# Performance work log

Hardware: AMD Instinct MI355X
Metric: run time of the kernel (lower is better)

The kernel has to match this reference:

```python
import jax, jax.numpy as jnp
import numpy as np

B, D = 32, 2048


def setup_inputs() -> dict:
    key = jax.random.key(0)
    ks = jax.random.split(key, 7)
    # torch init: weights ~ N(0, 0.1^2); biases default Linear uniform(-1/sqrt(D), 1/sqrt(D))
    bound = 1.0 / np.sqrt(D)
    return {
        "x": jax.random.normal(ks[0], (B, D), dtype=jnp.float32),
        "Wq": 0.1 * jax.random.normal(ks[1], (D, D), dtype=jnp.float32),
        "bq": jax.random.uniform(ks[2], (D,), minval=-bound, maxval=bound, dtype=jnp.float32),
        "Wk": 0.1 * jax.random.normal(ks[3], (D, D), dtype=jnp.float32),
        "bk": jax.random.uniform(ks[4], (D,), minval=-bound, maxval=bound, dtype=jnp.float32),
        "Wv": 0.1 * jax.random.normal(ks[5], (D, D), dtype=jnp.float32),
        "bv": jax.random.uniform(ks[6], (D,), minval=-bound, maxval=bound, dtype=jnp.float32),
    }


def reference(x, Wq, bq, Wk, bk, Wv, bv):
    # q,k,v: [B, D] feature-wise projections (torch Linear: x @ W^T + b)
    q = x @ Wq.T + bq
    k = x @ Wk.T + bk
    v = x @ Wv.T + bv
    # rank-1 outer product scores[b,i,j] = q[b,i] * k[b,j]  -> [B, D, D]
    scores = q[:, :, None] * k[:, None, :]
    # softmax over dim=1 (as in the original F.softmax(..., dim=1))
    weights = jax.nn.softmax(scores, axis=1)
    # weighted V sum: out[b,i] = sum_j weights[b,i,j] * v[b,j]  -> [B, D]
    out = jnp.einsum("bij,bj->bi", weights, v)
    return out
```

## Files before the change

kernel.cpp:

```cpp
#include <hip/hip_runtime.h>
#include <math.h>


#define D 2048
#define BATCH 32
#define SEGF 68
#define NPART 4

#define PART_STRIDE 196608
#define KDP_OFF 786432
#define NP_OFF  925696

#define L2E 1.4426950408889634f

typedef short s16x8 __attribute__((ext_vector_type(8)));
typedef float f32x4 __attribute__((ext_vector_type(4)));

union FragU { s16x8 v; unsigned u[4]; };

__device__ __forceinline__ float fast_exp2(float x) {
#if __has_builtin(__builtin_amdgcn_exp2f)
  return __builtin_amdgcn_exp2f(x);
#else
  return exp2f(x);
#endif
}
__device__ __forceinline__ unsigned pack_rne(float a, float b) {
  unsigned ua = __float_as_uint(a), ub = __float_as_uint(b);
  ua = ua + 0x7FFFu + ((ua >> 16) & 1u);
  ub = ub + 0x7FFFu + ((ub >> 16) & 1u);
  return (ua >> 16) | (ub & 0xFFFF0000u);
}
__device__ __forceinline__ void pack8(const float4& fa, const float4& fb,
                                      FragU& h) {
  h.u[0] = pack_rne(fa.x, fa.y);
  h.u[1] = pack_rne(fa.z, fa.w);
  h.u[2] = pack_rne(fb.x, fb.y);
  h.u[3] = pack_rne(fb.z, fb.w);
}
__device__ __forceinline__ float sum_parts(const float* __restrict__ ws,
                                           size_t o) {
  float s0 = ws[o] + ws[o + PART_STRIDE];
  float s1 = ws[o + 2 * PART_STRIDE] + ws[o + 3 * PART_STRIDE];
  return s0 + s1;
}

__global__ __launch_bounds__(256, 2) void k1_proj(
    const float* __restrict__ x, const float* __restrict__ Wq,
    const float* __restrict__ Wk, const float* __restrict__ Wv,
    float* __restrict__ ws) {
  __shared__ float red[4][512];
  const int tid = threadIdx.x;
  const int lane = tid & 63, wv = tid >> 6;
  const int tile = blockIdx.x >> 2, kq = blockIdx.x & 3;
  const int m = tile >> 7, lr = (tile & 127) * 16;
  const float* W = (m == 0) ? Wq : (m == 1) ? Wk : Wv;

  const int kbase = kq * 512 + wv * 128 + (lane >> 4) * 8;
  const float* ap = W + (size_t)(lr + (lane & 15)) * D + kbase;
  const float* xp0 = x + (size_t)(lane & 15) * D + kbase;
  const float* xp1 = xp0 + 16 * D;

  float4 fa[4], fb[4], x0a[4], x0b[4], x1a[4], x1b[4];
#pragma unroll
  for (int s = 0; s < 4; ++s) {
    const int off = s * 32;
    fa[s] = *(const float4*)(ap + off);
    fb[s] = *(const float4*)(ap + off + 4);
    x0a[s] = *(const float4*)(xp0 + off);
    x0b[s] = *(const float4*)(xp0 + off + 4);
    x1a[s] = *(const float4*)(xp1 + off);
    x1b[s] = *(const float4*)(xp1 + off + 4);
  }

  f32x4 acc0 = {0.f, 0.f, 0.f, 0.f}, acc1 = {0.f, 0.f, 0.f, 0.f};
#pragma unroll
  for (int s = 0; s < 4; ++s) {
    FragU Ah, Bh0, Bh1;
    pack8(fa[s], fb[s], Ah);
    pack8(x0a[s], x0b[s], Bh0);
    pack8(x1a[s], x1b[s], Bh1);
    acc0 = __builtin_amdgcn_mfma_f32_16x16x32_bf16(Ah.v, Bh0.v, acc0, 0, 0, 0);
    acc1 = __builtin_amdgcn_mfma_f32_16x16x32_bf16(Ah.v, Bh1.v, acc1, 0, 0, 0);
  }
  const int col = lane & 15, rq = (lane >> 4) * 4;
#pragma unroll
  for (int r = 0; r < 4; ++r) {
    red[wv][col * 16 + rq + r] = acc0[r];
    red[wv][(col + 16) * 16 + rq + r] = acc1[r];
  }
  __syncthreads();
  float* part = ws + (size_t)kq * PART_STRIDE + (size_t)m * 65536;
#pragma unroll
  for (int i = tid; i < 512; i += 256) {
    float s = (red[0][i] + red[1][i]) + (red[2][i] + red[3][i]);
    part[(size_t)(i >> 4) * D + lr + (i & 15)] = s;
  }
}

__global__ __launch_bounds__(512, 8) void k3_dz(float* __restrict__ ws,
                                                const float* __restrict__ bq,
                                                const float* __restrict__ bk,
                                                const float* __restrict__ bv) {
  __shared__ float qs[2048];
  __shared__ float zs[512];
  __shared__ float rmx[8], rmn[8];
  __shared__ int cnt[2];
  const int bx = blockIdx.x, t = threadIdx.x;
  const int b = bx >> 5, jc = bx & 31;
  if (t == 0) { cnt[0] = 0; cnt[1] = 0; }

  const size_t qb = (size_t)b * D;
  float4 p0 = ((const float4*)(ws + qb))[t];
  float4 p1 = ((const float4*)(ws + PART_STRIDE + qb))[t];
  float4 p2 = ((const float4*)(ws + 2 * PART_STRIDE + qb))[t];
  float4 p3 = ((const float4*)(ws + 3 * PART_STRIDE + qb))[t];
  float4 bb = ((const float4*)bq)[t];
  float4 qv = {(p0.x + p1.x) + (p2.x + p3.x) + bb.x,
               (p0.y + p1.y) + (p2.y + p3.y) + bb.y,
               (p0.z + p1.z) + (p2.z + p3.z) + bb.z,
               (p0.w + p1.w) + (p2.w + p3.w) + bb.w};
  *(float4*)&qs[t * 4] = qv;
  float mx = fmaxf(fmaxf(qv.x, qv.y), fmaxf(qv.z, qv.w));
  float mn = fminf(fminf(qv.x, qv.y), fminf(qv.z, qv.w));
#pragma unroll
  for (int off = 32; off; off >>= 1) {
    mx = fmaxf(mx, __shfl_down(mx, off));
    mn = fminf(mn, __shfl_down(mn, off));
  }
  if ((t & 63) == 0) { rmx[t >> 6] = mx; rmn[t >> 6] = mn; }
  __syncthreads();
  mx = rmx[0]; mn = rmn[0];
#pragma unroll
  for (int w = 1; w < 8; ++w) {
    mx = fmaxf(mx, rmx[w]);
    mn = fminf(mn, rmn[w]);
  }

  const int jl = t & 63, ih = t >> 6;
  const int j = jc * 64 + jl;
  const float k2 = (sum_parts(ws, 65536 + qb + j) + bk[j]) * L2E;
  const float m2 = (k2 >= 0.f) ? k2 * mx : k2 * mn;
  const float nm2 = -m2;
  const float* qp = qs + ih * 256;
  float z0 = 0.f, z1 = 0.f, z2 = 0.f, z3 = 0.f;
#pragma unroll 8
  for (int i = 0; i < 256; i += 4) {
    float4 q4 = *(const float4*)&qp[i];
    z0 += fast_exp2(fmaf(q4.x, k2, nm2));
    z1 += fast_exp2(fmaf(q4.y, k2, nm2));
    z2 += fast_exp2(fmaf(q4.z, k2, nm2));
    z3 += fast_exp2(fmaf(q4.w, k2, nm2));
  }
  zs[t] = (z0 + z1) + (z2 + z3);
  __syncthreads();

  float2* kdp = (float2*)(ws + KDP_OFF) + ((size_t)b * 32 + jc) * SEGF;
  if (t < 64) {
    float Z = ((zs[t] + zs[t + 64]) + (zs[t + 128] + zs[t + 192])) +
              ((zs[t + 256] + zs[t + 320]) + (zs[t + 384] + zs[t + 448]));
    float v = sum_parts(ws, 131072 + qb + j) + bv[j];
    float d = __log2f(fabsf(v) / Z) - m2;
    int slot;
    if (v >= 0.f) slot = atomicAdd(&cnt[0], 1);
    else          slot = (SEGF - 1) - atomicAdd(&cnt[1], 1);
    kdp[slot] = make_float2(k2, d);
  }
  __syncthreads();
  const int npos = cnt[0];
  if (t < 4) kdp[npos + t] = make_float2(0.f, -1e30f);
  if (t == 0) ((int*)(ws + NP_OFF))[b * 32 + jc] = npos;
}

__global__ __launch_bounds__(512, 8) void k4_out(const float* __restrict__ ws,
                                                 const float* __restrict__ bq,
                                                 float* __restrict__ out) {
  __shared__ float2 kd[32 * SEGF];
  __shared__ int np[32];
  __shared__ float rs[512];
  const int bx = blockIdx.x, t = threadIdx.x;
  const int b = bx >> 5, ic = bx & 31;

  const float4* src = (const float4*)((const float2*)(ws + KDP_OFF) +
                                      (size_t)b * 32 * SEGF);
  for (int idx = t; idx < (32 * SEGF) / 2; idx += 512)
    ((float4*)kd)[idx] = src[idx];
  if (t < 32) np[t] = ((const int*)(ws + NP_OFF))[b * 32 + t];

  const int il = t & 63, jh = t >> 6;
  const int i = ic * 64 + il;
  const size_t io = (size_t)b * D + i;
  const float qi = sum_parts(ws, io) + bq[i];
  __syncthreads();

  float p0 = 0.f, p1 = 0.f, p2 = 0.f, p3 = 0.f;
  float n0 = 0.f, n1 = 0.f, n2 = 0.f, n3 = 0.f;
#pragma unroll
  for (int s = jh * 4; s < jh * 4 + 4; ++s) {
    const float2* seg = kd + s * SEGF;
    const int npos = np[s];
    const int pe = (npos + 3) & ~3;
    const int ns = (npos + 4) & ~3;
    for (int jj = 0; jj < pe; jj += 4) {
      float4 t0 = *(const float4*)&seg[jj];
      float4 t1 = *(const float4*)&seg[jj + 2];
      p0 += fast_exp2(fmaf(qi, t0.x, t0.y));
      p1 += fast_exp2(fmaf(qi, t0.z, t0.w));
      p2 += fast_exp2(fmaf(qi, t1.x, t1.y));
      p3 += fast_exp2(fmaf(qi, t1.z, t1.w));
    }
    for (int jj = ns; jj < SEGF; jj += 4) {
      float4 t0 = *(const float4*)&seg[jj];
      float4 t1 = *(const float4*)&seg[jj + 2];
      n0 += fast_exp2(fmaf(qi, t0.x, t0.y));
      n1 += fast_exp2(fmaf(qi, t0.z, t0.w));
      n2 += fast_exp2(fmaf(qi, t1.x, t1.y));
      n3 += fast_exp2(fmaf(qi, t1.z, t1.w));
    }
  }
  rs[t] = ((p0 + p1) + (p2 + p3)) - ((n0 + n1) + (n2 + n3));
  __syncthreads();
  if (t < 64)
    out[io] = ((rs[il] + rs[il + 64]) + (rs[il + 128] + rs[il + 192])) +
              ((rs[il + 256] + rs[il + 320]) + (rs[il + 384] + rs[il + 448]));
}

extern "C" void kernel_launch(void* const* d_in, const int* in_sizes, int n_in,
                              void* d_out, int out_size, void* d_ws, size_t ws_size,
                              hipStream_t stream) {
  (void)in_sizes; (void)n_in; (void)out_size; (void)ws_size;
  const float* x  = (const float*)d_in[0];
  const float* Wq = (const float*)d_in[1];
  const float* bq = (const float*)d_in[2];
  const float* Wk = (const float*)d_in[3];
  const float* bk = (const float*)d_in[4];
  const float* Wv = (const float*)d_in[5];
  const float* bv = (const float*)d_in[6];
  float* ws  = (float*)d_ws;
  float* out = (float*)d_out;

  k1_proj<<<1536, 256, 0, stream>>>(x, Wq, Wk, Wv, ws);
  k3_dz<<<1024, 512, 0, stream>>>(ws, bq, bk, bv);
  k4_out<<<1024, 512, 0, stream>>>(ws, bq, out);
}
```

Measured before the change: 141.6 us.

## Finalize projections once and compact sign-split key lists per batch globally

A new k2_fin kernel sums the four split-K partials and adds the biases once, writing final q, scaled k and v. It also writes per-chunk q max/min so later kernels no longer re-reduce partials. k3 now appends (k,d) pairs into per-batch positive and negative global arrays using global atomic counters, replacing padded per-segment slots of 68 entries. k4 streams these compact lists straight from global memory with a uniform loop split across waves, removing the LDS staging and the padding waste. The cost is an extra kernel launch, contended global atomics, and cache reads in place of LDS in the hot exp loop.

```diff
diff --git a/kernel.cpp b/kernel.cpp
--- a/kernel.cpp
+++ b/kernel.cpp
@@ -4,12 +4,16 @@
 
 #define D 2048
 #define BATCH 32
-#define SEGF 68
 #define NPART 4
 
 #define PART_STRIDE 196608
-#define KDP_OFF 786432
-#define NP_OFF  925696
+#define QF_OFF  786432
+#define KF_OFF  851968
+#define VF_OFF  917504
+#define QMM_OFF 983040
+#define CNT_OFF 983552
+#define PKD_OFF 983616
+#define NKD_OFF 1114688
 
 #define L2E 1.4426950408889634f
 
@@ -37,12 +41,6 @@
   h.u[1] = pack_rne(fa.z, fa.w);
   h.u[2] = pack_rne(fb.x, fb.y);
   h.u[3] = pack_rne(fb.z, fb.w);
-}
-__device__ __forceinline__ float sum_parts(const float* __restrict__ ws,
-                                           size_t o) {
-  float s0 = ws[o] + ws[o + PART_STRIDE];
-  float s1 = ws[o + 2 * PART_STRIDE] + ws[o + 3 * PART_STRIDE];
-  return s0 + s1;
 }
 
 __global__ __launch_bounds__(256, 2) void k1_proj(
@@ -98,55 +96,68 @@
   }
 }
 
-__global__ __launch_bounds__(512, 8) void k3_dz(float* __restrict__ ws,
-                                                const float* __restrict__ bq,
-                                                const float* __restrict__ bk,
-                                                const float* __restrict__ bv) {
-  __shared__ float qs[2048];
+__global__ __launch_bounds__(256) void k2_fin(float* __restrict__ ws,
+                                              const float* __restrict__ bq,
+                                              const float* __restrict__ bk,
+                                              const float* __restrict__ bv) {
+  __shared__ float smx[4], smn[4];
+  const int id = blockIdx.x, t = threadIdx.x;
+  const int m = id >> 8, r = id & 255, b = r >> 3, c = r & 7;
+  const int i = c * 256 + t;
+  const size_t e = (size_t)m * 65536 + (size_t)b * D + i;
+  float s = (ws[e] + ws[e + PART_STRIDE]) +
+            (ws[e + 2 * PART_STRIDE] + ws[e + 3 * PART_STRIDE]);
+  if (m == 0) {
+    s += bq[i];
+    ws[QF_OFF + (size_t)b * D + i] = s;
+    float mx = s, mn = s;
+#pragma unroll
+    for (int off = 32; off; off >>= 1) {
+      mx = fmaxf(mx, __shfl_down(mx, off));
+      mn = fminf(mn, __shfl_down(mn, off));
+    }
+    if ((t & 63) == 0) { smx[t >> 6] = mx; smn[t >> 6] = mn; }
+    __syncthreads();
+    if (t == 0) {
+      mx = fmaxf(fmaxf(smx[0], smx[1]), fmaxf(smx[2], smx[3]));
+      mn = fminf(fminf(smn[0], smn[1]), fminf(smn[2], smn[3]));
+      float* qm = ws + QMM_OFF + (size_t)(b * 8 + c) * 2;
+      qm[0] = mx; qm[1] = mn;
+    }
+    if (c == 0 && t < 2) ((int*)(ws + CNT_OFF))[b * 2 + t] = 0;
+  } else if (m == 1) {
+    ws[KF_OFF + (size_t)b * D + i] = (s + bk[i]) * L2E;
+  } else {
+    ws[VF_OFF + (size_t)b * D + i] = s + bv[i];
+  }
+}
+
+__global__ __launch_bounds__(512, 8) void k3_z(
+    const float* __restrict__ qf, const float* __restrict__ kf,
+    const float* __restrict__ vf, const float* __restrict__ qmm,
+    int* __restrict__ cnt, float2* __restrict__ pkd,
+    float2* __restrict__ nkd) {
   __shared__ float zs[512];
-  __shared__ float rmx[8], rmn[8];
-  __shared__ int cnt[2];
   const int bx = blockIdx.x, t = threadIdx.x;
   const int b = bx >> 5, jc = bx & 31;
-  if (t == 0) { cnt[0] = 0; cnt[1] = 0; }
-
-  const size_t qb = (size_t)b * D;
-  float4 p0 = ((const float4*)(ws + qb))[t];
-  float4 p1 = ((const float4*)(ws + PART_STRIDE + qb))[t];
-  float4 p2 = ((const float4*)(ws + 2 * PART_STRIDE + qb))[t];
-  float4 p3 = ((const float4*)(ws + 3 * PART_STRIDE + qb))[t];
-  float4 bb = ((const float4*)bq)[t];
-  float4 qv = {(p0.x + p1.x) + (p2.x + p3.x) + bb.x,
-               (p0.y + p1.y) + (p2.y + p3.y) + bb.y,
-               (p0.z + p1.z) + (p2.z + p3.z) + bb.z,
-               (p0.w + p1.w) + (p2.w + p3.w) + bb.w};
-  *(float4*)&qs[t * 4] = qv;
-  float mx = fmaxf(fmaxf(qv.x, qv.y), fmaxf(qv.z, qv.w));
-  float mn = fminf(fminf(qv.x, qv.y), fminf(qv.z, qv.w));
-#pragma unroll
-  for (int off = 32; off; off >>= 1) {
-    mx = fmaxf(mx, __shfl_down(mx, off));
-    mn = fminf(mn, __shfl_down(mn, off));
-  }
-  if ((t & 63) == 0) { rmx[t >> 6] = mx; rmn[t >> 6] = mn; }
-  __syncthreads();
-  mx = rmx[0]; mn = rmn[0];
+  const int jl = t & 63;
+  const int ih = __builtin_amdgcn_readfirstlane(t >> 6);
+  const int j = jc * 64 + jl;
+  const float k2 = kf[(size_t)b * D + j];
+  const float* qm = qmm + b * 16;
+  float mx = qm[0], mn = qm[1];
 #pragma unroll
   for (int w = 1; w < 8; ++w) {
-    mx = fmaxf(mx, rmx[w]);
-    mn = fminf(mn, rmn[w]);
-  }
-
-  const int jl = t & 63, ih = t >> 6;
-  const int j = jc * 64 + jl;
-  const float k2 = (sum_parts(ws, 65536 + qb + j) + bk[j]) * L2E;
+    mx = fmaxf(mx, qm[2 * w]);
+    mn = fminf(mn, qm[2 * w + 1]);
+  }
   const float m2 = (k2 >= 0.f) ? k2 * mx : k2 * mn;
   const float nm2 = -m2;
-  const float* qp = qs + ih * 256;
+  const float* qp = qf + (size_t)b * D + ih * 256;
   float z0 = 0.f, z1 = 0.f, z2 = 0.f, z3 = 0.f;
 #pragma unroll 8
-  for (int i = 0; i < 256; i += 4) {
-    float4 q4 = *(const float4*)&qp[i];
+  for (int i2 = 0; i2 < 256; i2 += 4) {
+    float4 q4 = *(const float4*)(qp + i2);
     z0 += fast_exp2(fmaf(q4.x, k2, nm2));
     z1 += fast_exp2(fmaf(q4.y, k2, nm2));
     z2 += fast_exp2(fmaf(q4.z, k2, nm2));
@@ -154,75 +165,74 @@
   }
   zs[t] = (z0 + z1) + (z2 + z3);
   __syncthreads();
-
-  float2* kdp = (float2*)(ws + KDP_OFF) + ((size_t)b * 32 + jc) * SEGF;
   if (t < 64) {
     float Z = ((zs[t] + zs[t + 64]) + (zs[t + 128] + zs[t + 192])) +
               ((zs[t + 256] + zs[t + 320]) + (zs[t + 384] + zs[t + 448]));
-    float v = sum_parts(ws, 131072 + qb + j) + bv[j];
-    float d = __log2f(fabsf(v) / Z) - m2;
-    int slot;
-    if (v >= 0.f) slot = atomicAdd(&cnt[0], 1);
-    else          slot = (SEGF - 1) - atomicAdd(&cnt[1], 1);
-    kdp[slot] = make_float2(k2, d);
-  }
-  __syncthreads();
-  const int npos = cnt[0];
-  if (t < 4) kdp[npos + t] = make_float2(0.f, -1e30f);
-  if (t == 0) ((int*)(ws + NP_OFF))[b * 32 + jc] = npos;
-}
-
-__global__ __launch_bounds__(512, 8) void k4_out(const float* __restrict__ ws,
-                                                 const float* __restrict__ bq,
-                                                 float* __restrict__ out) {
-  __shared__ float2 kd[32 * SEGF];
-  __shared__ int np[32];
+    const float v = vf[(size_t)b * D + j];
+    const float d = __log2f(fabsf(v) / Z) - m2;
+    if (v >= 0.f) {
+      int s = atomicAdd(&cnt[b * 2], 1);
+      pkd[(size_t)b * D + s] = make_float2(k2, d);
+    } else {
+      int s = atomicAdd(&cnt[b * 2 + 1], 1);
+      nkd[(size_t)b * D + s] = make_float2(k2, d);
+    }
+  }
+}
+
+__global__ __launch_bounds__(512, 8) void k4_out(
+    const float* __restrict__ qf, const int* __restrict__ cnt,
+    const float2* __restrict__ pkd, const float2* __restrict__ nkd,
+    float* __restrict__ out) {
   __shared__ float rs[512];
   const int bx = blockIdx.x, t = threadIdx.x;
   const int b = bx >> 5, ic = bx & 31;
-
-  const float4* src = (const float4*)((const float2*)(ws + KDP_OFF) +
-                                      (size_t)b * 32 * SEGF);
-  for (int idx = t; idx < (32 * SEGF) / 2; idx += 512)
-    ((float4*)kd)[idx] = src[idx];
-  if (t < 32) np[t] = ((const int*)(ws + NP_OFF))[b * 32 + t];
-
-  const int il = t & 63, jh = t >> 6;
+  const int il = t & 63;
+  const int jh = __builtin_amdgcn_readfirstlane(t >> 6);
   const int i = ic * 64 + il;
-  const size_t io = (size_t)b * D + i;
-  const float qi = sum_parts(ws, io) + bq[i];
-  __syncthreads();
+  const float qi = qf[(size_t)b * D + i];
+  const int npos = cnt[b * 2], nneg = cnt[b * 2 + 1];
+  const float2* pp = pkd + (size_t)b * D;
+  const float2* np = nkd + (size_t)b * D;
 
   float p0 = 0.f, p1 = 0.f, p2 = 0.f, p3 = 0.f;
+  const int GP = npos >> 2;
+  for (int g = jh; g < GP; g += 8) {
+    const float4* e4 = (const float4*)(pp + g * 4);
+    float4 a = e4[0], c4 = e4[1];
+    p0 += fast_exp2(fmaf(qi, a.x, a.y));
+    p1 += fast_exp2(fmaf(qi, a.z, a.w));
+    p2 += fast_exp2(fmaf(qi, c4.x, c4.y));
+    p3 += fast_exp2(fmaf(qi, c4.z, c4.w));
+  }
+  if (jh == 0) {
+    for (int jj = GP * 4; jj < npos; ++jj) {
+      float2 e = pp[jj];
+      p0 += fast_exp2(fmaf(qi, e.x, e.y));
+    }
+  }
   float n0 = 0.f, n1 = 0.f, n2 = 0.f, n3 = 0.f;
-#pragma unroll
-  for (int s = jh * 4; s < jh * 4 + 4; ++s) {
-    const float2* seg = kd + s * SEGF;
-    const int npos = np[s];
-    const int pe = (npos + 3) & ~3;
-    const int ns = (npos + 4) & ~3;
-    for (int jj = 0; jj < pe; jj += 4) {
-      float4 t0 = *(const float4*)&seg[jj];
-      float4 t1 = *(const float4*)&seg[jj + 2];
-      p0 += fast_exp2(fmaf(qi, t0.x, t0.y));
-      p1 += fast_exp2(fmaf(qi, t0.z, t0.w));
-      p2 += fast_exp2(fmaf(qi, t1.x, t1.y));
-      p3 += fast_exp2(fmaf(qi, t1.z, t1.w));
-    }
-    for (int jj = ns; jj < SEGF; jj += 4) {
-      float4 t0 = *(const float4*)&seg[jj];
-      float4 t1 = *(const float4*)&seg[jj + 2];
-      n0 += fast_exp2(fmaf(qi, t0.x, t0.y));
-      n1 += fast_exp2(fmaf(qi, t0.z, t0.w));
-      n2 += fast_exp2(fmaf(qi, t1.x, t1.y));
-      n3 += fast_exp2(fmaf(qi, t1.z, t1.w));
+  const int GN = nneg >> 2;
+  for (int g = jh; g < GN; g += 8) {
+    const float4* e4 = (const float4*)(np + g * 4);
+    float4 a = e4[0], c4 = e4[1];
+    n0 += fast_exp2(fmaf(qi, a.x, a.y));
+    n1 += fast_exp2(fmaf(qi, a.z, a.w));
+    n2 += fast_exp2(fmaf(qi, c4.x, c4.y));
+    n3 += fast_exp2(fmaf(qi, c4.z, c4.w));
+  }
+  if (jh == 1) {
+    for (int jj = GN * 4; jj < nneg; ++jj) {
+      float2 e = np[jj];
+      n0 += fast_exp2(fmaf(qi, e.x, e.y));
     }
   }
   rs[t] = ((p0 + p1) + (p2 + p3)) - ((n0 + n1) + (n2 + n3));
   __syncthreads();
   if (t < 64)
-    out[io] = ((rs[il] + rs[il + 64]) + (rs[il + 128] + rs[il + 192])) +
-              ((rs[il + 256] + rs[il + 320]) + (rs[il + 384] + rs[il + 448]));
+    out[(size_t)b * D + ic * 64 + t] =
+        ((rs[t] + rs[t + 64]) + (rs[t + 128] + rs[t + 192])) +
+        ((rs[t + 256] + rs[t + 320]) + (rs[t + 384] + rs[t + 448]));
 }
 
 extern "C" void kernel_launch(void* const* d_in, const int* in_sizes, int n_in,
@@ -240,6 +250,12 @@
   float* out = (float*)d_out;
 
   k1_proj<<<1536, 256, 0, stream>>>(x, Wq, Wk, Wv, ws);
-  k3_dz<<<1024, 512, 0, stream>>>(ws, bq, bk, bv);
-  k4_out<<<1024, 512, 0, stream>>>(ws, bq, out);
-}
+  k2_fin<<<768, 256, 0, stream>>>(ws, bq, bk, bv);
+  k3_z<<<1024, 512, 0, stream>>>(ws + QF_OFF, ws + KF_OFF, ws + VF_OFF,
+                                 ws + QMM_OFF, (int*)(ws + CNT_OFF),
+                                 (float2*)(ws + PKD_OFF),
+                                 (float2*)(ws + NKD_OFF));
+  k4_out<<<1024, 512, 0, stream>>>(ws + QF_OFF, (const int*)(ws + CNT_OFF),
+                                   (const float2*)(ws + PKD_OFF),
+                                   (const float2*)(ws + NKD_OFF), out);
+}
```

Result: slower. 544.6 us (+284.6%).

## Register-block two columns per thread and compact sign-partitioned k/d segments

Applied to the files above, without the earlier changes.

The Z kernel now has each thread handle two j columns, so each shared q load feeds two exp pipelines. Positive/negative partitioning uses a wavefront ballot with mbcnt instead of LDS atomics, writing 64-entry segments with no padding sentinels. The output kernel processes two i rows per thread over half as many blocks, reusing each LDS k/d load for both rows and handling the single mixed group with per-element predication. This cuts LDS traffic per exp and removes atomics, at the cost of more registers and lower declared occupancy in k4.

```diff
diff --git a/kernel.cpp b/kernel.cpp
--- a/kernel.cpp
+++ b/kernel.cpp
@@ -4,12 +4,11 @@
 
 #define D 2048
 #define BATCH 32
-#define SEGF 68
 #define NPART 4
 
 #define PART_STRIDE 196608
-#define KDP_OFF 786432
-#define NP_OFF  925696
+#define PKD_OFF 786432
+#define NPT_OFF 917504
 
 #define L2E 1.4426950408889634f
 
@@ -24,6 +23,10 @@
 #else
   return exp2f(x);
 #endif
+}
+__device__ __forceinline__ int bits_below(unsigned long long m) {
+  return __builtin_amdgcn_mbcnt_hi((unsigned)(m >> 32),
+         __builtin_amdgcn_mbcnt_lo((unsigned)m, 0));
 }
 __device__ __forceinline__ unsigned pack_rne(float a, float b) {
   unsigned ua = __float_as_uint(a), ub = __float_as_uint(b);
@@ -98,19 +101,18 @@
   }
 }
 
-__global__ __launch_bounds__(512, 8) void k3_dz(float* __restrict__ ws,
-                                                const float* __restrict__ bq,
-                                                const float* __restrict__ bk,
-                                                const float* __restrict__ bv) {
+__global__ __launch_bounds__(512, 8) void k3_z(float* __restrict__ ws,
+                                               const float* __restrict__ bq,
+                                               const float* __restrict__ bk,
+                                               const float* __restrict__ bv) {
   __shared__ float qs[2048];
-  __shared__ float zs[512];
+  __shared__ float zs[1024];
+  __shared__ float ks2[64], ms2[64];
   __shared__ float rmx[8], rmn[8];
-  __shared__ int cnt[2];
   const int bx = blockIdx.x, t = threadIdx.x;
   const int b = bx >> 5, jc = bx & 31;
-  if (t == 0) { cnt[0] = 0; cnt[1] = 0; }
-
   const size_t qb = (size_t)b * D;
+
   float4 p0 = ((const float4*)(ws + qb))[t];
   float4 p1 = ((const float4*)(ws + PART_STRIDE + qb))[t];
   float4 p2 = ((const float4*)(ws + 2 * PART_STRIDE + qb))[t];
@@ -137,92 +139,138 @@
     mn = fminf(mn, rmn[w]);
   }
 
-  const int jl = t & 63, ih = t >> 6;
-  const int j = jc * 64 + jl;
-  const float k2 = (sum_parts(ws, 65536 + qb + j) + bk[j]) * L2E;
-  const float m2 = (k2 >= 0.f) ? k2 * mx : k2 * mn;
-  const float nm2 = -m2;
-  const float* qp = qs + ih * 256;
-  float z0 = 0.f, z1 = 0.f, z2 = 0.f, z3 = 0.f;
+  const int jp = t & 31, ih = t >> 5;
+  const int j0 = jc * 64 + jp, j1 = j0 + 32;
+  const float k2a = (sum_parts(ws, 65536 + qb + j0) + bk[j0]) * L2E;
+  const float k2b = (sum_parts(ws, 65536 + qb + j1) + bk[j1]) * L2E;
+  const float m2a = (k2a >= 0.f) ? k2a * mx : k2a * mn;
+  const float m2b = (k2b >= 0.f) ? k2b * mx : k2b * mn;
+  if (ih == 0) {
+    ks2[jp] = k2a; ks2[32 + jp] = k2b;
+    ms2[jp] = m2a; ms2[32 + jp] = m2b;
+  }
+  const float na = -m2a, nb = -m2b;
+  const float* qp = qs + ih * 128;
+  float za0 = 0.f, za1 = 0.f, za2 = 0.f, za3 = 0.f;
+  float zb0 = 0.f, zb1 = 0.f, zb2 = 0.f, zb3 = 0.f;
 #pragma unroll 8
-  for (int i = 0; i < 256; i += 4) {
-    float4 q4 = *(const float4*)&qp[i];
-    z0 += fast_exp2(fmaf(q4.x, k2, nm2));
-    z1 += fast_exp2(fmaf(q4.y, k2, nm2));
-    z2 += fast_exp2(fmaf(q4.z, k2, nm2));
-    z3 += fast_exp2(fmaf(q4.w, k2, nm2));
-  }
-  zs[t] = (z0 + z1) + (z2 + z3);
-  __syncthreads();
-
-  float2* kdp = (float2*)(ws + KDP_OFF) + ((size_t)b * 32 + jc) * SEGF;
+  for (int i2 = 0; i2 < 128; i2 += 4) {
+    float4 q4 = *(const float4*)&qp[i2];
+    za0 += fast_exp2(fmaf(q4.x, k2a, na));
+    za1 += fast_exp2(fmaf(q4.y, k2a, na));
+    za2 += fast_exp2(fmaf(q4.z, k2a, na));
+    za3 += fast_exp2(fmaf(q4.w, k2a, na));
+    zb0 += fast_exp2(fmaf(q4.x, k2b, nb));
+    zb1 += fast_exp2(fmaf(q4.y, k2b, nb));
+    zb2 += fast_exp2(fmaf(q4.z, k2b, nb));
+    zb3 += fast_exp2(fmaf(q4.w, k2b, nb));
+  }
+  zs[ih * 64 + jp]      = (za0 + za1) + (za2 + za3);
+  zs[ih * 64 + 32 + jp] = (zb0 + zb1) + (zb2 + zb3);
+  __syncthreads();
+
   if (t < 64) {
-    float Z = ((zs[t] + zs[t + 64]) + (zs[t + 128] + zs[t + 192])) +
-              ((zs[t + 256] + zs[t + 320]) + (zs[t + 384] + zs[t + 448]));
-    float v = sum_parts(ws, 131072 + qb + j) + bv[j];
-    float d = __log2f(fabsf(v) / Z) - m2;
-    int slot;
-    if (v >= 0.f) slot = atomicAdd(&cnt[0], 1);
-    else          slot = (SEGF - 1) - atomicAdd(&cnt[1], 1);
-    kdp[slot] = make_float2(k2, d);
-  }
-  __syncthreads();
-  const int npos = cnt[0];
-  if (t < 4) kdp[npos + t] = make_float2(0.f, -1e30f);
-  if (t == 0) ((int*)(ws + NP_OFF))[b * 32 + jc] = npos;
-}
-
-__global__ __launch_bounds__(512, 8) void k4_out(const float* __restrict__ ws,
+    float Z = 0.f;
+#pragma unroll
+    for (int h = 0; h < 16; ++h) Z += zs[h * 64 + t];
+    const int j = jc * 64 + t;
+    const float v = sum_parts(ws, 131072 + qb + j) + bv[j];
+    const float d = __log2f(fabsf(v) / Z) - ms2[t];
+    const unsigned long long msk = __ballot(v >= 0.f);
+    const int npos = __popcll(msk);
+    const int slot = (v >= 0.f) ? bits_below(msk) : 63 - bits_below(~msk);
+    float2* dst = (float2*)(ws + PKD_OFF) + ((size_t)b * 32 + jc) * 64;
+    dst[slot] = make_float2(ks2[t], d);
+    if (t == 0) ((int*)(ws + NPT_OFF))[b * 32 + jc] = npos;
+  }
+}
+
+__global__ __launch_bounds__(512, 4) void k4_out(const float* __restrict__ ws,
                                                  const float* __restrict__ bq,
                                                  float* __restrict__ out) {
-  __shared__ float2 kd[32 * SEGF];
+  __shared__ float2 kd[2048];
   __shared__ int np[32];
-  __shared__ float rs[512];
+  __shared__ float rs[128 * 9];
   const int bx = blockIdx.x, t = threadIdx.x;
-  const int b = bx >> 5, ic = bx & 31;
-
-  const float4* src = (const float4*)((const float2*)(ws + KDP_OFF) +
-                                      (size_t)b * 32 * SEGF);
-  for (int idx = t; idx < (32 * SEGF) / 2; idx += 512)
-    ((float4*)kd)[idx] = src[idx];
-  if (t < 32) np[t] = ((const int*)(ws + NP_OFF))[b * 32 + t];
+  const int b = bx >> 4, ic = bx & 15;
+  const size_t qb = (size_t)b * D;
+
+  const float4* src = (const float4*)((const float2*)(ws + PKD_OFF) +
+                                      (size_t)b * 2048);
+  ((float4*)kd)[t] = src[t];
+  ((float4*)kd)[t + 512] = src[t + 512];
+  if (t < 32) np[t] = ((const int*)(ws + NPT_OFF))[b * 32 + t];
 
   const int il = t & 63, jh = t >> 6;
-  const int i = ic * 64 + il;
-  const size_t io = (size_t)b * D + i;
-  const float qi = sum_parts(ws, io) + bq[i];
-  __syncthreads();
-
-  float p0 = 0.f, p1 = 0.f, p2 = 0.f, p3 = 0.f;
-  float n0 = 0.f, n1 = 0.f, n2 = 0.f, n3 = 0.f;
-#pragma unroll
-  for (int s = jh * 4; s < jh * 4 + 4; ++s) {
-    const float2* seg = kd + s * SEGF;
-    const int npos = np[s];
-    const int pe = (npos + 3) & ~3;
-    const int ns = (npos + 4) & ~3;
-    for (int jj = 0; jj < pe; jj += 4) {
-      float4 t0 = *(const float4*)&seg[jj];
-      float4 t1 = *(const float4*)&seg[jj + 2];
-      p0 += fast_exp2(fmaf(qi, t0.x, t0.y));
-      p1 += fast_exp2(fmaf(qi, t0.z, t0.w));
-      p2 += fast_exp2(fmaf(qi, t1.x, t1.y));
-      p3 += fast_exp2(fmaf(qi, t1.z, t1.w));
+  const int i0 = ic * 128 + il, i1 = i0 + 64;
+  const float qi0 = sum_parts(ws, qb + i0) + bq[i0];
+  const float qi1 = sum_parts(ws, qb + i1) + bq[i1];
+  __syncthreads();
+
+  float pa0 = 0.f, pa1 = 0.f, pa2 = 0.f, pa3 = 0.f;
+  float pb0 = 0.f, pb1 = 0.f, pb2 = 0.f, pb3 = 0.f;
+  float na0 = 0.f, na1 = 0.f, na2 = 0.f, na3 = 0.f;
+  float nb0 = 0.f, nb1 = 0.f, nb2 = 0.f, nb3 = 0.f;
+#pragma unroll
+  for (int s4 = 0; s4 < 4; ++s4) {
+    const int s = jh * 4 + s4;
+    const float4* seg = (const float4*)(kd + s * 64);
+    const int npos = np[s], gb = npos >> 2;
+    for (int g = 0; g < gb; ++g) {
+      float4 a = seg[g * 2], c = seg[g * 2 + 1];
+      pa0 += fast_exp2(fmaf(qi0, a.x, a.y));
+      pa1 += fast_exp2(fmaf(qi0, a.z, a.w));
+      pa2 += fast_exp2(fmaf(qi0, c.x, c.y));
+      pa3 += fast_exp2(fmaf(qi0, c.z, c.w));
+      pb0 += fast_exp2(fmaf(qi1, a.x, a.y));
+      pb1 += fast_exp2(fmaf(qi1, a.z, a.w));
+      pb2 += fast_exp2(fmaf(qi1, c.x, c.y));
+      pb3 += fast_exp2(fmaf(qi1, c.z, c.w));
     }
-    for (int jj = ns; jj < SEGF; jj += 4) {
-      float4 t0 = *(const float4*)&seg[jj];
-      float4 t1 = *(const float4*)&seg[jj + 2];
-      n0 += fast_exp2(fmaf(qi, t0.x, t0.y));
-      n1 += fast_exp2(fmaf(qi, t0.z, t0.w));
-      n2 += fast_exp2(fmaf(qi, t1.x, t1.y));
-      n3 += fast_exp2(fmaf(qi, t1.z, t1.w));
+    if (gb < 16) {
+      {
+        float4 a = seg[gb * 2], c = seg[gb * 2 + 1];
+        const int base = gb * 4;
+        float ea0 = fast_exp2(fmaf(qi0, a.x, a.y));
+        float ea1 = fast_exp2(fmaf(qi0, a.z, a.w));
+        float ea2 = fast_exp2(fmaf(qi0, c.x, c.y));
+        float ea3 = fast_exp2(fmaf(qi0, c.z, c.w));
+        float eb0 = fast_exp2(fmaf(qi1, a.x, a.y));
+        float eb1 = fast_exp2(fmaf(qi1, a.z, a.w));
+        float eb2 = fast_exp2(fmaf(qi1, c.x, c.y));
+        float eb3 = fast_exp2(fmaf(qi1, c.z, c.w));
+        if (base + 0 < npos) { pa0 += ea0; pb0 += eb0; }
+        else                 { na0 += ea0; nb0 += eb0; }
+        if (base + 1 < npos) { pa1 += ea1; pb1 += eb1; }
+        else                 { na1 += ea1; nb1 += eb1; }
+        if (base + 2 < npos) { pa2 += ea2; pb2 += eb2; }
+        else                 { na2 += ea2; nb2 += eb2; }
+        if (base + 3 < npos) { pa3 += ea3; pb3 += eb3; }
+        else                 { na3 += ea3; nb3 += eb3; }
+      }
+      for (int g = gb + 1; g < 16; ++g) {
+        float4 a = seg[g * 2], c = seg[g * 2 + 1];
+        na0 += fast_exp2(fmaf(qi0, a.x, a.y));
+        na1 += fast_exp2(fmaf(qi0, a.z, a.w));
+        na2 += fast_exp2(fmaf(qi0, c.x, c.y));
+        na3 += fast_exp2(fmaf(qi0, c.z, c.w));
+        nb0 += fast_exp2(fmaf(qi1, a.x, a.y));
+        nb1 += fast_exp2(fmaf(qi1, a.z, a.w));
+        nb2 += fast_exp2(fmaf(qi1, c.x, c.y));
+        nb3 += fast_exp2(fmaf(qi1, c.z, c.w));
+      }
     }
   }
-  rs[t] = ((p0 + p1) + (p2 + p3)) - ((n0 + n1) + (n2 + n3));
-  __syncthreads();
-  if (t < 64)
-    out[io] = ((rs[il] + rs[il + 64]) + (rs[il + 128] + rs[il + 192])) +
-              ((rs[il + 256] + rs[il + 320]) + (rs[il + 384] + rs[il + 448]));
+  rs[il * 9 + jh] = ((pa0 + pa1) + (pa2 + pa3)) - ((na0 + na1) + (na2 + na3));
+  rs[(64 + il) * 9 + jh] =
+      ((pb0 + pb1) + (pb2 + pb3)) - ((nb0 + nb1) + (nb2 + nb3));
+  __syncthreads();
+  if (t < 128) {
+    float s = 0.f;
+#pragma unroll
+    for (int h = 0; h < 8; ++h) s += rs[t * 9 + h];
+    out[qb + ic * 128 + t] = s;
+  }
 }
 
 extern "C" void kernel_launch(void* const* d_in, const int* in_sizes, int n_in,
@@ -240,6 +288,6 @@
   float* out = (float*)d_out;
 
   k1_proj<<<1536, 256, 0, stream>>>(x, Wq, Wk, Wv, ws);
-  k3_dz<<<1024, 512, 0, stream>>>(ws, bq, bk, bv);
-  k4_out<<<1024, 512, 0, stream>>>(ws, bq, out);
-}
+  k3_z<<<1024, 512, 0, stream>>>(ws, bq, bk, bv);
+  k4_out<<<512, 512, 0, stream>>>(ws, bq, out);
+}
```

Result: no change. 140.2 us (-1.0%).

## Bucket-sort q and k per batch to skip negligible exp terms in softmax

Applied to the files above, without the earlier changes.

Adds a prep kernel that bucket-sorts q and scaled k values per batch into 64 value bins. The Z kernel then only sums exp terms over the q range that can exceed 2^-40 relative to the max. The output kernel groups k by sorted order and skips whole 32-element segments whose upper bound falls below 2^-28. This removes most of the exp evaluations, but it adds an extra launch, a scatter to original indices, and a numerical truncation that depends on the data distribution.

```diff
diff --git a/kernel.cpp b/kernel.cpp
--- a/kernel.cpp
+++ b/kernel.cpp
@@ -4,12 +4,16 @@
 
 #define D 2048
 #define BATCH 32
-#define SEGF 68
-#define NPART 4
 
 #define PART_STRIDE 196608
-#define KDP_OFF 786432
-#define NP_OFF  925696
+#define BQV_OFF   786432
+#define BQI_OFF   851968
+#define BK2_OFF   917504
+#define BKI_OFF   983040
+#define META_OFF  1048576
+#define PKD_OFF   1051136
+#define NPT_OFF   1182208
+#define SMETA_OFF 1184256
 
 #define L2E 1.4426950408889634f
 
@@ -24,6 +28,10 @@
 #else
   return exp2f(x);
 #endif
+}
+__device__ __forceinline__ int bits_below(unsigned long long m) {
+  return __builtin_amdgcn_mbcnt_hi((unsigned)(m >> 32),
+         __builtin_amdgcn_mbcnt_lo((unsigned)m, 0));
 }
 __device__ __forceinline__ unsigned pack_rne(float a, float b) {
   unsigned ua = __float_as_uint(a), ub = __float_as_uint(b);
@@ -98,37 +106,38 @@
   }
 }
 
-__global__ __launch_bounds__(512, 8) void k3_dz(float* __restrict__ ws,
-                                                const float* __restrict__ bq,
-                                                const float* __restrict__ bk,
-                                                const float* __restrict__ bv) {
-  __shared__ float qs[2048];
-  __shared__ float zs[512];
+__global__ __launch_bounds__(512) void k0_prep(float* __restrict__ ws,
+                                               const float* __restrict__ bq,
+                                               const float* __restrict__ bk) {
+  __shared__ int cnt[64], off[65], cur[64];
   __shared__ float rmx[8], rmn[8];
-  __shared__ int cnt[2];
   const int bx = blockIdx.x, t = threadIdx.x;
-  const int b = bx >> 5, jc = bx & 31;
-  if (t == 0) { cnt[0] = 0; cnt[1] = 0; }
-
+  const int b = bx & 31, pass = bx >> 5;
   const size_t qb = (size_t)b * D;
-  float4 p0 = ((const float4*)(ws + qb))[t];
-  float4 p1 = ((const float4*)(ws + PART_STRIDE + qb))[t];
-  float4 p2 = ((const float4*)(ws + 2 * PART_STRIDE + qb))[t];
-  float4 p3 = ((const float4*)(ws + 3 * PART_STRIDE + qb))[t];
-  float4 bb = ((const float4*)bq)[t];
+  float* meta = ws + META_OFF + b * 80;
+
+  const size_t src = (pass ? 65536 : 0) + qb;
+  float4 p0 = ((const float4*)(ws + src))[t];
+  float4 p1 = ((const float4*)(ws + PART_STRIDE + src))[t];
+  float4 p2 = ((const float4*)(ws + 2 * PART_STRIDE + src))[t];
+  float4 p3 = ((const float4*)(ws + 3 * PART_STRIDE + src))[t];
+  float4 bb = pass ? ((const float4*)bk)[t] : ((const float4*)bq)[t];
   float4 qv = {(p0.x + p1.x) + (p2.x + p3.x) + bb.x,
                (p0.y + p1.y) + (p2.y + p3.y) + bb.y,
                (p0.z + p1.z) + (p2.z + p3.z) + bb.z,
                (p0.w + p1.w) + (p2.w + p3.w) + bb.w};
-  *(float4*)&qs[t * 4] = qv;
+  if (pass) {
+    qv.x *= L2E; qv.y *= L2E; qv.z *= L2E; qv.w *= L2E;
+  }
   float mx = fmaxf(fmaxf(qv.x, qv.y), fmaxf(qv.z, qv.w));
   float mn = fminf(fminf(qv.x, qv.y), fminf(qv.z, qv.w));
 #pragma unroll
-  for (int off = 32; off; off >>= 1) {
-    mx = fmaxf(mx, __shfl_down(mx, off));
-    mn = fminf(mn, __shfl_down(mn, off));
+  for (int o = 32; o; o >>= 1) {
+    mx = fmaxf(mx, __shfl_down(mx, o));
+    mn = fminf(mn, __shfl_down(mn, o));
   }
   if ((t & 63) == 0) { rmx[t >> 6] = mx; rmn[t >> 6] = mn; }
+  if (t < 64) cnt[t] = 0;
   __syncthreads();
   mx = rmx[0]; mn = rmn[0];
 #pragma unroll
@@ -136,93 +145,181 @@
     mx = fmaxf(mx, rmx[w]);
     mn = fminf(mn, rmn[w]);
   }
-
-  const int jl = t & 63, ih = t >> 6;
-  const int j = jc * 64 + jl;
-  const float k2 = (sum_parts(ws, 65536 + qb + j) + bk[j]) * L2E;
-  const float m2 = (k2 >= 0.f) ? k2 * mx : k2 * mn;
+  const float scale = (mx > mn) ? 64.0f / (mx - mn) : 0.f;
+  float vals[4] = {qv.x, qv.y, qv.z, qv.w};
+  int bi[4];
+#pragma unroll
+  for (int e = 0; e < 4; ++e) {
+    bi[e] = (int)fminf(63.f, fmaxf(0.f, (vals[e] - mn) * scale));
+    atomicAdd(&cnt[bi[e]], 1);
+  }
+  __syncthreads();
+  if (t == 0) {
+    int a = 0;
+#pragma unroll
+    for (int i = 0; i < 64; ++i) { off[i] = a; cur[i] = a; a += cnt[i]; }
+    off[64] = a;
+  }
+  __syncthreads();
+  const size_t vdst = (pass ? BK2_OFF : BQV_OFF) + qb;
+  const size_t idst = (pass ? BKI_OFF : BQI_OFF) + qb;
+#pragma unroll
+  for (int e = 0; e < 4; ++e) {
+    const int pos = atomicAdd(&cur[bi[e]], 1);
+    ws[vdst + pos] = vals[e];
+    ((int*)ws)[idst + pos] = t * 4 + e;
+  }
+  if (pass == 0) {
+    if (t == 0) { meta[0] = mx; meta[1] = mn; meta[2] = scale; }
+    if (t < 65) ((int*)meta)[8 + t] = off[t];
+  }
+}
+
+__global__ __launch_bounds__(512, 8) void k3_z(float* __restrict__ ws,
+                                               const float* __restrict__ bv) {
+  __shared__ float qs[2048];
+  __shared__ float zs[512];
+  __shared__ int ob[65];
+  const int bx = blockIdx.x, t = threadIdx.x;
+  const int b = bx & 31, s = bx >> 5;
+  const int g = (s & 1) ? 32 + (s >> 1) : 31 - (s >> 1);
+  const size_t qb = (size_t)b * D;
+  const float* meta = ws + META_OFF + b * 80;
+
+  ((float4*)qs)[t] = ((const float4*)(ws + BQV_OFF + qb))[t];
+  if (t < 65) ob[t] = ((const int*)meta)[8 + t];
+  const float qmx = meta[0], qmn = meta[1], scale = meta[2];
+
+  const int jl = t & 31, ih = t >> 5;
+  const int p = g * 32 + jl;
+  const float k2 = ws[BK2_OFF + qb + p];
+  const int oj = ((const int*)ws)[BKI_OFF + qb + p];
+  const float m2 = (k2 >= 0.f) ? k2 * qmx : k2 * qmn;
   const float nm2 = -m2;
-  const float* qp = qs + ih * 256;
+  __syncthreads();
+
+  int st, en;
+  if (k2 >= 0.f) {
+    const float c = qmx - 40.f / k2;
+    const int B = (int)fminf(63.f, fmaxf(0.f, (c - qmn) * scale));
+    st = ob[B] & ~3; en = 2048;
+  } else {
+    const float c = qmn + 40.f / (-k2);
+    const int B = (int)fminf(63.f, fmaxf(0.f, (c - qmn) * scale));
+    st = 0; en = (ob[B + 1] + 3) & ~3;
+  }
+  const int nq = (en - st) >> 2;
+  const int i0 = st + (((nq * ih) >> 4) << 2);
+  const int i1 = st + (((nq * (ih + 1)) >> 4) << 2);
   float z0 = 0.f, z1 = 0.f, z2 = 0.f, z3 = 0.f;
-#pragma unroll 8
-  for (int i = 0; i < 256; i += 4) {
-    float4 q4 = *(const float4*)&qp[i];
+  for (int idx = i0; idx < i1; idx += 4) {
+    float4 q4 = *(const float4*)&qs[idx];
     z0 += fast_exp2(fmaf(q4.x, k2, nm2));
     z1 += fast_exp2(fmaf(q4.y, k2, nm2));
     z2 += fast_exp2(fmaf(q4.z, k2, nm2));
     z3 += fast_exp2(fmaf(q4.w, k2, nm2));
   }
-  zs[t] = (z0 + z1) + (z2 + z3);
-  __syncthreads();
-
-  float2* kdp = (float2*)(ws + KDP_OFF) + ((size_t)b * 32 + jc) * SEGF;
+  zs[ih * 32 + jl] = (z0 + z1) + (z2 + z3);
+  __syncthreads();
+
+  if (t < 32) {
+    float Z = 0.f;
+#pragma unroll
+    for (int h = 0; h < 16; ++h) Z += zs[h * 32 + t];
+    const float v = sum_parts(ws, 131072 + qb + oj) + bv[oj];
+    const float d = __log2f(fabsf(v) / Z) - m2;
+    const unsigned long long msk = __ballot(v >= 0.f);
+    const int npos = __popcll(msk);
+    const int slot = (v >= 0.f) ? bits_below(msk)
+                                : 31 - bits_below(~msk & 0xFFFFFFFFull);
+    float2* dst = (float2*)(ws + PKD_OFF) + ((size_t)b * 64 + g) * 32;
+    dst[slot] = make_float2(k2, d);
+    if (t == 0) ((int*)(ws + NPT_OFF))[b * 64 + g] = npos;
+    float kmn = k2, kmx = k2, dmx = d;
+#pragma unroll
+    for (int o = 16; o; o >>= 1) {
+      kmn = fminf(kmn, __shfl_down(kmn, o, 32));
+      kmx = fmaxf(kmx, __shfl_down(kmx, o, 32));
+      dmx = fmaxf(dmx, __shfl_down(dmx, o, 32));
+    }
+    if (t == 0)
+      ((float4*)(ws + SMETA_OFF))[b * 64 + g] =
+          make_float4(kmn, kmx, dmx, 0.f);
+  }
+}
+
+__global__ __launch_bounds__(512, 8) void k4_out(const float* __restrict__ ws,
+                                                 float* __restrict__ out) {
+  __shared__ float2 kd[2048];
+  __shared__ float4 sm[64];
+  __shared__ int np[64];
+  __shared__ float rs[32 * 17];
+  const int bx = blockIdx.x, t = threadIdx.x;
+  const int b = bx & 31, s = bx >> 5;
+  const int ic = (s & 1) ? 63 - (s >> 1) : (s >> 1);
+  const size_t qb = (size_t)b * D;
+
+  const float4* src = (const float4*)((const float2*)(ws + PKD_OFF) +
+                                      (size_t)b * 2048);
+  ((float4*)kd)[t] = src[t];
+  ((float4*)kd)[t + 512] = src[t + 512];
   if (t < 64) {
-    float Z = ((zs[t] + zs[t + 64]) + (zs[t + 128] + zs[t + 192])) +
-              ((zs[t + 256] + zs[t + 320]) + (zs[t + 384] + zs[t + 448]));
-    float v = sum_parts(ws, 131072 + qb + j) + bv[j];
-    float d = __log2f(fabsf(v) / Z) - m2;
-    int slot;
-    if (v >= 0.f) slot = atomicAdd(&cnt[0], 1);
-    else          slot = (SEGF - 1) - atomicAdd(&cnt[1], 1);
-    kdp[slot] = make_float2(k2, d);
-  }
-  __syncthreads();
-  const int npos = cnt[0];
-  if (t < 4) kdp[npos + t] = make_float2(0.f, -1e30f);
-  if (t == 0) ((int*)(ws + NP_OFF))[b * 32 + jc] = npos;
-}
-
-__global__ __launch_bounds__(512, 8) void k4_out(const float* __restrict__ ws,
-                                                 const float* __restrict__ bq,
-                                                 float* __restrict__ out) {
-  __shared__ float2 kd[32 * SEGF];
-  __shared__ int np[32];
-  __shared__ float rs[512];
-  const int bx = blockIdx.x, t = threadIdx.x;
-  const int b = bx >> 5, ic = bx & 31;
-
-  const float4* src = (const float4*)((const float2*)(ws + KDP_OFF) +
-                                      (size_t)b * 32 * SEGF);
-  for (int idx = t; idx < (32 * SEGF) / 2; idx += 512)
-    ((float4*)kd)[idx] = src[idx];
-  if (t < 32) np[t] = ((const int*)(ws + NP_OFF))[b * 32 + t];
-
-  const int il = t & 63, jh = t >> 6;
-  const int i = ic * 64 + il;
-  const size_t io = (size_t)b * D + i;
-  const float qi = sum_parts(ws, io) + bq[i];
+    np[t] = ((const int*)(ws + NPT_OFF))[b * 64 + t];
+    sm[t] = ((const float4*)(ws + SMETA_OFF))[b * 64 + t];
+  }
+  const int il = t & 31, jh = t >> 5;
+  const int pos = ic * 32 + il;
+  const float qi = ws[BQV_OFF + qb + pos];
+  const int oi = ((const int*)ws)[BQI_OFF + qb + pos];
   __syncthreads();
 
   float p0 = 0.f, p1 = 0.f, p2 = 0.f, p3 = 0.f;
   float n0 = 0.f, n1 = 0.f, n2 = 0.f, n3 = 0.f;
 #pragma unroll
-  for (int s = jh * 4; s < jh * 4 + 4; ++s) {
-    const float2* seg = kd + s * SEGF;
-    const int npos = np[s];
-    const int pe = (npos + 3) & ~3;
-    const int ns = (npos + 4) & ~3;
-    for (int jj = 0; jj < pe; jj += 4) {
-      float4 t0 = *(const float4*)&seg[jj];
-      float4 t1 = *(const float4*)&seg[jj + 2];
-      p0 += fast_exp2(fmaf(qi, t0.x, t0.y));
-      p1 += fast_exp2(fmaf(qi, t0.z, t0.w));
-      p2 += fast_exp2(fmaf(qi, t1.x, t1.y));
-      p3 += fast_exp2(fmaf(qi, t1.z, t1.w));
+  for (int s4 = 0; s4 < 4; ++s4) {
+    const int sg = jh * 4 + s4;
+    const float4 m = sm[sg];
+    const float ub = fmaxf(m.x * qi, m.y * qi) + m.z;
+    if (ub < -28.f) continue;
+    const float4* seg = (const float4*)(kd + sg * 32);
+    const int npos = np[sg], gb = npos >> 2;
+    for (int gq = 0; gq < gb; ++gq) {
+      float4 a = seg[gq * 2], c = seg[gq * 2 + 1];
+      p0 += fast_exp2(fmaf(qi, a.x, a.y));
+      p1 += fast_exp2(fmaf(qi, a.z, a.w));
+      p2 += fast_exp2(fmaf(qi, c.x, c.y));
+      p3 += fast_exp2(fmaf(qi, c.z, c.w));
     }
-    for (int jj = ns; jj < SEGF; jj += 4) {
-      float4 t0 = *(const float4*)&seg[jj];
-      float4 t1 = *(const float4*)&seg[jj + 2];
-      n0 += fast_exp2(fmaf(qi, t0.x, t0.y));
-      n1 += fast_exp2(fmaf(qi, t0.z, t0.w));
-      n2 += fast_exp2(fmaf(qi, t1.x, t1.y));
-      n3 += fast_exp2(fmaf(qi, t1.z, t1.w));
+    if (gb < 8) {
+      {
+        float4 a = seg[gb * 2], c = seg[gb * 2 + 1];
+        const int base = gb * 4;
+        float e0 = fast_exp2(fmaf(qi, a.x, a.y));
+        float e1 = fast_exp2(fmaf(qi, a.z, a.w));
+        float e2 = fast_exp2(fmaf(qi, c.x, c.y));
+        float e3 = fast_exp2(fmaf(qi, c.z, c.w));
+        if (base + 0 < npos) p0 += e0; else n0 += e0;
+        if (base + 1 < npos) p1 += e1; else n1 += e1;
+        if (base + 2 < npos) p2 += e2; else n2 += e2;
+        if (base + 3 < npos) p3 += e3; else n3 += e3;
+      }
+      for (int gq = gb + 1; gq < 8; ++gq) {
+        float4 a = seg[gq * 2], c = seg[gq * 2 + 1];
+        n0 += fast_exp2(fmaf(qi, a.x, a.y));
+        n1 += fast_exp2(fmaf(qi, a.z, a.w));
+        n2 += fast_exp2(fmaf(qi, c.x, c.y));
+        n3 += fast_exp2(fmaf(qi, c.z, c.w));
+      }
     }
   }
-  rs[t] = ((p0 + p1) + (p2 + p3)) - ((n0 + n1) + (n2 + n3));
-  __syncthreads();
-  if (t < 64)
-    out[io] = ((rs[il] + rs[il + 64]) + (rs[il + 128] + rs[il + 192])) +
-              ((rs[il + 256] + rs[il + 320]) + (rs[il + 384] + rs[il + 448]));
+  rs[il * 17 + jh] = ((p0 + p1) + (p2 + p3)) - ((n0 + n1) + (n2 + n3));
+  __syncthreads();
+  if (t < 32) {
+    float sum = 0.f;
+#pragma unroll
+    for (int h = 0; h < 16; ++h) sum += rs[t * 17 + h];
+    out[qb + oi] = sum;
+  }
 }
 
 extern "C" void kernel_launch(void* const* d_in, const int* in_sizes, int n_in,
@@ -240,6 +337,7 @@
   float* out = (float*)d_out;
 
   k1_proj<<<1536, 256, 0, stream>>>(x, Wq, Wk, Wv, ws);
-  k3_dz<<<1024, 512, 0, stream>>>(ws, bq, bk, bv);
-  k4_out<<<1024, 512, 0, stream>>>(ws, bq, out);
-}
+  k0_prep<<<64, 512, 0, stream>>>(ws, bq, bk);
+  k3_z<<<2048, 512, 0, stream>>>(ws, bv);
+  k4_out<<<2048, 512, 0, stream>>>(ws, out);
+}
```

Measured after the change: 136.5 us. 3.6% less time.
